# Kernel tuning notes

Measured on AMD Instinct MI355X. Metric: run time of the kernel, lower is better.

The kernel has to match this reference:

```python
import jax, jax.numpy as jnp
import numpy as np
import math

N_HEAD = 16

def setup_inputs() -> dict:
    key = jax.random.key(0)
    ks = jax.random.split(key, 8)
    B, S, P, NX = 4, 1024, 128, 1024
    return {
        "x": jax.random.normal(ks[0], (B, S, NX), jnp.float32),
        "M": jax.random.normal(ks[1], (B, P, NX), jnp.float32),
        "Mmask": jnp.ones((B, P), jnp.float32),
        "attention_mask": jnp.zeros((B, 1, 1, S), jnp.float32),
        "W_attn": jax.random.normal(ks[2], (NX, 3 * NX), jnp.float32) * 0.02,
        "b_attn": jnp.zeros((3 * NX,), jnp.float32),
        "W_mem": jax.random.normal(ks[3], (NX, 2 * NX), jnp.float32) * 0.02,
        "b_mem": jnp.zeros((2 * NX,), jnp.float32),
        "W_proj": jax.random.normal(ks[4], (NX, NX), jnp.float32) * 0.02,
        "b_proj": jnp.zeros((NX,), jnp.float32),
    }

def _split_heads(t, H):
    B, T, NX = t.shape
    return t.reshape(B, T, H, NX // H).transpose(0, 2, 1, 3)  # [B,H,T,dh]

def reference(x, M, Mmask, attention_mask, W_attn, b_attn, W_mem, b_mem, W_proj, b_proj):
    B, S, NX = x.shape
    H = N_HEAD
    dh = NX // H
    P = M.shape[1]

    # fused QKV projection (Conv1D == x @ W + b)
    qkv = x @ W_attn + b_attn
    q, k, v = jnp.split(qkv, 3, axis=2)

    # memory K/V projection, prepended along the key/value sequence axis
    ekv = M @ W_mem + b_mem
    ek, ev = jnp.split(ekv, 2, axis=2)
    key = jnp.concatenate([ek, k], axis=1)   # [B, P+S, NX]
    value = jnp.concatenate([ev, v], axis=1)

    qh = _split_heads(q, H)      # [B,H,S,dh]
    kh = _split_heads(key, H)    # [B,H,P+S,dh]
    vh = _split_heads(value, H)  # [B,H,P+S,dh]

    w = jnp.einsum('bhsd,bhtd->bhst', qh, kh) / math.sqrt(dh)  # [B,H,S,P+S]

    # causal bias over the self part, all-ones over the memory part
    causal = jnp.tril(jnp.ones((S, S), w.dtype))
    b = jnp.concatenate([jnp.ones((S, P), w.dtype), causal], axis=1)[None, None]  # [1,1,S,P+S]
    w = w * b - 10000.0 * (1.0 - b)

    # additive attention mask: memory-mask bias concatenated before token mask
    mem_bias = (1.0 - Mmask)[:, None, None, :] * -10000.0  # [B,1,1,P]
    am = jnp.concatenate([mem_bias, jnp.broadcast_to(attention_mask, (B, 1, 1, S))], axis=3)
    w = w + am

    w = jax.nn.softmax(w, axis=-1)
    a = jnp.einsum('bhst,bhtd->bhsd', w, vh)                  # [B,H,S,dh]
    a = a.transpose(0, 2, 1, 3).reshape(B, S, NX)             # merge heads
    return a @ W_proj + b_proj
```

## Files before the change

kernel.cpp:

```cpp
#include <hip/hip_runtime.h>
#include <hip/hip_bf16.h>


typedef __attribute__((ext_vector_type(8))) short bf16x8;
typedef __attribute__((ext_vector_type(4))) float f32x4;

#define MFMA16(a, b, c) __builtin_amdgcn_mfma_f32_16x16x32_bf16((a), (b), (c), 0, 0, 0)

#define GLOAD_LDS16(g, l)                                                  \
    __builtin_amdgcn_global_load_lds(                                      \
        (const __attribute__((address_space(1))) void*)(const void*)(g),   \
        (__attribute__((address_space(3))) void*)(void*)(l), 16, 0, 0)

static __device__ __forceinline__ unsigned short f2bf(float f) {
    union { float f; unsigned int u; } v; v.f = f;
    unsigned int u = v.u;
    return (unsigned short)((u + 0x7fffu + ((u >> 16) & 1u)) >> 16);
}

static __device__ __forceinline__ void transpose64(const float* __restrict__ W,
                                                   unsigned short* __restrict__ Wt,
                                                   int K, int N, int bx, int by,
                                                   float* tile ) {
    const int n0 = bx * 64, k0 = by * 64;
    const int tr = threadIdx.x >> 2, tc = (threadIdx.x & 3) * 16;
    #pragma unroll
    for (int i = 0; i < 4; i++) {
        float4 v = *(const float4*)&W[(size_t)(k0 + tr) * N + n0 + tc + i * 4];
        tile[tr * 65 + tc + i * 4 + 0] = v.x;
        tile[tr * 65 + tc + i * 4 + 1] = v.y;
        tile[tr * 65 + tc + i * 4 + 2] = v.z;
        tile[tr * 65 + tc + i * 4 + 3] = v.w;
    }
    __syncthreads();
    union { ushort4 u4[2]; unsigned short s[8]; } pk[2];
    #pragma unroll
    for (int half = 0; half < 2; half++)
        #pragma unroll
        for (int i = 0; i < 8; i++)
            pk[half].s[i] = f2bf(tile[(tc + half * 8 + i) * 65 + tr]);
    unsigned short* dst = &Wt[(size_t)(n0 + tr) * K + k0 + tc];
    *(ushort4*)(dst + 0) = pk[0].u4[0];
    *(ushort4*)(dst + 4) = pk[0].u4[1];
    *(ushort4*)(dst + 8) = pk[1].u4[0];
    *(ushort4*)(dst + 12) = pk[1].u4[1];
}

__global__ void prep_all(const float* __restrict__ x, const float* __restrict__ Mem,
                         unsigned short* __restrict__ x_bf, unsigned short* __restrict__ M_bf,
                         const float* __restrict__ W_attn, const float* __restrict__ W_mem,
                         const float* __restrict__ W_proj, unsigned short* __restrict__ Wat,
                         unsigned short* __restrict__ Wmt, unsigned short* __restrict__ Wpt,
                         const float* __restrict__ Mmask, const float* __restrict__ amask,
                         float* __restrict__ biasT) {
    __shared__ float tile[64 * 65];
    int bid = blockIdx.x;
    if (bid < 4608) {
        int i = bid * 256 + threadIdx.x;
        if (i < 1048576) {
            float4 v = ((const float4*)x)[i];
            ushort4 o; o.x = f2bf(v.x); o.y = f2bf(v.y); o.z = f2bf(v.z); o.w = f2bf(v.w);
            ((ushort4*)x_bf)[i] = o;
        } else {
            int j = i - 1048576;
            float4 v = ((const float4*)Mem)[j];
            ushort4 o; o.x = f2bf(v.x); o.y = f2bf(v.y); o.z = f2bf(v.z); o.w = f2bf(v.w);
            ((ushort4*)M_bf)[j] = o;
        }
        return;
    }
    bid -= 4608;
    if (bid < 768) {
        transpose64(W_attn, Wat, 1024, 3072, bid % 48, bid / 48, tile);
    } else if (bid < 1280) {
        int t = bid - 768;  transpose64(W_mem, Wmt, 1024, 2048, t % 32, t / 32, tile);
    } else if (bid < 1536) {
        int t = bid - 1280; transpose64(W_proj, Wpt, 1024, 1024, t % 16, t / 16, tile);
    } else {
        int i = (bid - 1536) * 256 + threadIdx.x;
        if (i < 4 * 1152) {
            int b = i / 1152, t = i % 1152;
            float v = (t < 128) ? (Mmask[b * 128 + t] - 1.f) * 10000.f
                                : amask[b * 1024 + t - 128];
            biasT[i] = v * 1.4426950408889634f;
        }
    }
}

__global__ __launch_bounds__(256, 4) void gemm_fused(
        const unsigned short* __restrict__ x_bf, const unsigned short* __restrict__ Wat,
        const float* __restrict__ b_attn, const unsigned short* __restrict__ M_bf,
        const unsigned short* __restrict__ Wmt, const float* __restrict__ b_mem,
        unsigned short* __restrict__ Qbuf, unsigned short* __restrict__ Kc,
        unsigned short* __restrict__ Vt) {
    __shared__ char smem[34816];
    unsigned short* As = (unsigned short*)smem;
    unsigned short* Bs = (unsigned short*)(smem + 8192);
    const int tid = threadIdx.x;
    const int lane = tid & 63, wave = tid >> 6;
    const int quad = lane >> 4, l16 = lane & 15;
    const int crow = lane >> 2, ccol = (lane & 3) * 8;
    const int bid = blockIdx.x;

    if (bid < 768) {
        const int bm = bid & 31, bn = bid >> 5;
        const int wm = (wave & 1) * 64, wn = (wave >> 1) * 64;
        const unsigned short* Abase = x_bf + (size_t)(bm * 128 + crow) * 1024 + ccol;
        const unsigned short* Bbase = Wat + (size_t)(bn * 128 + crow) * 1024 + ccol;
        f32x4 acc[4][4] = {};
        for (int k0 = 0; k0 < 1024; k0 += 32) {
            __syncthreads();
            #pragma unroll
            for (int cc = 0; cc < 4; cc++) {
                const int c = wave * 4 + cc;
                if (c < 8) GLOAD_LDS16(Abase + (size_t)(c * 16) * 1024 + k0, &As[c * 512]);
                else       GLOAD_LDS16(Bbase + (size_t)((c - 8) * 16) * 1024 + k0, &Bs[(c - 8) * 512]);
            }
            __syncthreads();
            bf16x8 af[4], bf[4];
            #pragma unroll
            for (int i = 0; i < 4; i++) af[i] = *(const bf16x8*)&As[(wm + i * 16 + l16) * 32 + quad * 8];
            #pragma unroll
            for (int j = 0; j < 4; j++) bf[j] = *(const bf16x8*)&Bs[(wn + j * 16 + l16) * 32 + quad * 8];
            #pragma unroll
            for (int i = 0; i < 4; i++)
                #pragma unroll
                for (int j = 0; j < 4; j++)
                    acc[i][j] = MFMA16(af[i], bf[j], acc[i][j]);
        }
        float bj[4];
        #pragma unroll
        for (int j = 0; j < 4; j++) bj[j] = b_attn[bn * 128 + wn + j * 16 + l16];
        __syncthreads();
        if (bn < 8) {
            #pragma unroll
            for (int i = 0; i < 4; i++) {
                const int row = bm * 128 + wm + i * 16 + quad * 4;
                #pragma unroll
                for (int j = 0; j < 4; j++) {
                    const int col = bn * 128 + wn + j * 16 + l16;
                    #pragma unroll
                    for (int r = 0; r < 4; r++)
                        Qbuf[(size_t)(row + r) * 1024 + col] = f2bf(acc[i][j][r] + bj[j]);
                }
            }
        } else if (bn < 16) {
            #pragma unroll
            for (int i = 0; i < 4; i++) {
                const int row = bm * 128 + wm + i * 16 + quad * 4;
                const int b = row >> 10, s = row & 1023;
                #pragma unroll
                for (int j = 0; j < 4; j++) {
                    const int c = bn * 128 + wn + j * 16 + l16 - 1024;
                    unsigned short* kd = Kc + (size_t)((b << 4) | (c >> 6)) * 73728 +
                                         (size_t)(s + 128) * 64 + (c & 63);
                    #pragma unroll
                    for (int r = 0; r < 4; r++) kd[(size_t)r * 64] = f2bf(acc[i][j][r] + bj[j]);
                }
            }
        } else {
            unsigned short* Tw = (unsigned short*)smem + wave * 4352;
            #pragma unroll
            for (int i = 0; i < 4; i++)
                #pragma unroll
                for (int j = 0; j < 4; j++)
                    #pragma unroll
                    for (int r = 0; r < 4; r++)
                        Tw[(j * 16 + l16) * 68 + i * 16 + quad * 4 + r] = f2bf(acc[i][j][r] + bj[j]);
            const int vb = (bn - 16) * 128 + wn;
            const int h = vb >> 6;
            const int b = bm >> 3, s0 = (bm * 128 + wm) & 1023;
            unsigned short* vd = Vt + (size_t)((b << 4) | h) * 73728 +
                                 (size_t)lane * 1152 + 128 + s0;
            #pragma unroll
            for (int ch = 0; ch < 8; ch++)
                *(bf16x8*)(vd + ch * 8) = *(const bf16x8*)&Tw[lane * 68 + ch * 8];
        }
    } else {
        const int t = bid - 768;
        const int bm = t >> 5, bn = t & 31;
        const int wm = (wave & 1) * 32, wn = (wave >> 1) * 32;
        const unsigned short* Abase = M_bf + (size_t)(bm * 64 + crow) * 1024 + ccol;
        const unsigned short* Bbase = Wmt + (size_t)(bn * 64 + crow) * 1024 + ccol;
        f32x4 acc[2][2] = {};
        for (int k0 = 0; k0 < 1024; k0 += 32) {
            __syncthreads();
            #pragma unroll
            for (int cc = 0; cc < 2; cc++) {
                const int c = wave * 2 + cc;
                if (c < 4) GLOAD_LDS16(Abase + (size_t)(c * 16) * 1024 + k0, &As[c * 512]);
                else       GLOAD_LDS16(Bbase + (size_t)((c - 4) * 16) * 1024 + k0, &Bs[(c - 4) * 512]);
            }
            __syncthreads();
            bf16x8 af[2], bf[2];
            #pragma unroll
            for (int i = 0; i < 2; i++) af[i] = *(const bf16x8*)&As[(wm + i * 16 + l16) * 32 + quad * 8];
            #pragma unroll
            for (int j = 0; j < 2; j++) bf[j] = *(const bf16x8*)&Bs[(wn + j * 16 + l16) * 32 + quad * 8];
            #pragma unroll
            for (int i = 0; i < 2; i++)
                #pragma unroll
                for (int j = 0; j < 2; j++)
                    acc[i][j] = MFMA16(af[i], bf[j], acc[i][j]);
        }
        float bj[2];
        #pragma unroll
        for (int j = 0; j < 2; j++) bj[j] = b_mem[bn * 64 + wn + j * 16 + l16];
        __syncthreads();
        if (bn < 16) {
            #pragma unroll
            for (int i = 0; i < 2; i++) {
                const int row = bm * 64 + wm + i * 16 + quad * 4;
                const int b = row >> 7, p = row & 127;
                #pragma unroll
                for (int j = 0; j < 2; j++) {
                    const int c = bn * 64 + wn + j * 16 + l16;
                    unsigned short* kd = Kc + (size_t)((b << 4) | (c >> 6)) * 73728 +
                                         (size_t)p * 64 + (c & 63);
                    #pragma unroll
                    for (int r = 0; r < 4; r++) kd[(size_t)r * 64] = f2bf(acc[i][j][r] + bj[j]);
                }
            }
        } else {
            unsigned short* Tw = (unsigned short*)smem + wave * 1152;
            #pragma unroll
            for (int i = 0; i < 2; i++)
                #pragma unroll
                for (int j = 0; j < 2; j++)
                    #pragma unroll
                    for (int r = 0; r < 4; r++)
                        Tw[(j * 16 + l16) * 36 + i * 16 + quad * 4 + r] = f2bf(acc[i][j][r] + bj[j]);
            const int vb = bn * 64 + wn - 1024;
            const int h = vb >> 6, d0 = vb & 63;
            const int b = (bm * 64 + wm) >> 7, p0 = (bm * 64 + wm) & 127;
            const int lc = lane >> 1, half = lane & 1;
            unsigned short* vd = Vt + (size_t)((b << 4) | h) * 73728 +
                                 (size_t)(d0 + lc) * 1152 + p0 + half * 16;
            #pragma unroll
            for (int ch = 0; ch < 2; ch++)
                *(bf16x8*)(vd + ch * 8) = *(const bf16x8*)&Tw[lc * 36 + half * 16 + ch * 8];
        }
    }
}

__global__ __launch_bounds__(128) void attn_kernel(const unsigned short* __restrict__ Qbuf,
                                                   const unsigned short* __restrict__ Kc,
                                                   const unsigned short* __restrict__ Vt,
                                                   const float* __restrict__ biasT,
                                                   unsigned short* __restrict__ Aout) {
    __shared__ unsigned short Ks[2][64 * 64];
    __shared__ unsigned short Vs[2][64 * 64];
    __shared__ unsigned short Ps[2][16 * 72];
    const int tid = threadIdx.x;
    const int lane = tid & 63, wave = tid >> 6;
    const int quad = lane >> 4, l16 = lane & 15;
    const int blk = blockIdx.x;
    const int xcd = blk & 7, idx = blk >> 3;
    const int bh = xcd * 8 + (idx & 7);
    const int pair = idx >> 3;
    const int h = bh & 15, b = bh >> 4;

    const unsigned short* Kb = Kc + (size_t)bh * 73728;
    const unsigned short* Vb = Vt + (size_t)bh * 73728;
    const float* bias_b = biasT + b * 1152;

    const int srow = lane >> 3;
    const int scol = ((lane & 7) ^ srow) * 8;
    const int rswz = l16 & 7;
    const int w32 = wave * 32;

#define STAGE_KV(t0_, kdst_, vdst_)                                            \
    {                                                                          \
        const unsigned short* gk = Kb + (size_t)((t0_) + w32 + srow) * 64 + scol; \
        const unsigned short* gv = Vb + (size_t)(w32 + srow) * 1152 + (t0_) + scol; \
        _Pragma("unroll")                                                      \
        for (int cc = 0; cc < 4; cc++) {                                       \
            GLOAD_LDS16(gk + (size_t)(cc * 8) * 64,   &(kdst_)[(w32 + cc * 8) * 64]); \
            GLOAD_LDS16(gv + (size_t)(cc * 8) * 1152, &(vdst_)[(w32 + cc * 8) * 64]); \
        }                                                                      \
    }

    bf16x8 ones;
    #pragma unroll
    for (int j = 0; j < 8; j++) ones[j] = (short)0x3F80;

    #pragma unroll
    for (int phase = 0; phase < 2; phase++) {
        const int qg = phase ? (31 - pair) : pair;
        const int qrow0 = qg * 32;
        const int qrow_w = qrow0 + wave * 16;

        bf16x8 qf[2];
        #pragma unroll
        for (int k2 = 0; k2 < 2; k2++)
            qf[k2] = *(const bf16x8*)(Qbuf + (size_t)(b * 1024 + qrow_w + l16) * 1024 +
                                      h * 64 + k2 * 32 + quad * 8);

        f32x4 o[4] = {};
        f32x4 oden = {};
        const int tmax = min(1152, ((qrow0 + 223) >> 6) << 6);

        STAGE_KV(0, Ks[0], Vs[0]);

        for (int t0 = 0; t0 < tmax; t0 += 64) {
            const int cur = (t0 >> 6) & 1;
            if (t0 + 64 < tmax) {
                if (cur) { STAGE_KV(t0 + 64, Ks[0], Vs[0]); }
                else     { STAGE_KV(t0 + 64, Ks[1], Vs[1]); }
                asm volatile("s_waitcnt vmcnt(8)\n\ts_barrier" ::: "memory");
            } else {
                asm volatile("s_waitcnt vmcnt(0)\n\ts_barrier" ::: "memory");
            }
            if (t0 <= qrow_w + 143) {
                const unsigned short* Kcur = Ks[cur];
                const unsigned short* Vcur = Vs[cur];
                const bool nomask = (t0 + 63 <= 128 + qrow_w);
                float4 bt[4];
                #pragma unroll
                for (int tn = 0; tn < 4; tn++)
                    bt[tn] = *(const float4*)(bias_b + t0 + tn * 16 + quad * 4);
                const int sg = qrow_w + l16;
                #pragma unroll
                for (int tn = 0; tn < 4; tn++) {
                    bf16x8 kf0 = *(const bf16x8*)&Kcur[(tn * 16 + l16) * 64 + (quad ^ rswz) * 8];
                    bf16x8 kf1 = *(const bf16x8*)&Kcur[(tn * 16 + l16) * 64 + ((quad + 4) ^ rswz) * 8];
                    f32x4 st = {};
                    st = MFMA16(kf0, qf[0], st);
                    st = MFMA16(kf1, qf[1], st);
                    float p[4];
                    #pragma unroll
                    for (int r = 0; r < 4; r++) {
                        float e = __builtin_amdgcn_exp2f(st[r] * 0.18033688011112042f + bt[tn][r]);
                        if (!nomask) {
                            const int tg = t0 + tn * 16 + quad * 4 + r;
                            e = (tg < 128 || tg - 128 <= sg) ? e : 0.f;
                        }
                        p[r] = e;
                    }
                    union { ushort4 u; __hip_bfloat162 h2[2]; } pk;
                    pk.h2[0] = __float22bfloat162_rn(float2{p[0], p[1]});
                    pk.h2[1] = __float22bfloat162_rn(float2{p[2], p[3]});
                    *(ushort4*)&Ps[wave][l16 * 72 + tn * 16 + quad * 4] = pk.u;
                }
                #pragma unroll
                for (int tk = 0; tk < 2; tk++) {
                    bf16x8 pf = *(const bf16x8*)&Ps[wave][l16 * 72 + tk * 32 + quad * 8];
                    oden = MFMA16(pf, ones, oden);
                    #pragma unroll
                    for (int dn = 0; dn < 4; dn++) {
                        bf16x8 vf = *(const bf16x8*)&Vcur[(dn * 16 + l16) * 64 +
                                                          ((tk * 4 + quad) ^ rswz) * 8];
                        o[dn] = MFMA16(pf, vf, o[dn]);
                    }
                }
            }
            asm volatile("s_barrier" ::: "memory");
        }

        #pragma unroll
        for (int r = 0; r < 4; r++) {
            const float inv = 1.f / oden[r];
            const size_t orow = (size_t)(b * 1024 + qrow_w + quad * 4 + r) * 1024 + h * 64;
            #pragma unroll
            for (int dn = 0; dn < 4; dn++)
                Aout[orow + dn * 16 + l16] = f2bf(o[dn][r] * inv);
        }
    }
#undef STAGE_KV
}

__global__ __launch_bounds__(256) void gemm_proj(const unsigned short* __restrict__ Abuf,
                                                 const unsigned short* __restrict__ Wpt,
                                                 const float* __restrict__ b_proj,
                                                 float* __restrict__ out) {
    __shared__ unsigned short As[128 * 32];
    __shared__ unsigned short Bs[64 * 32];
    const int tid = threadIdx.x;
    const int lane = tid & 63, wave = tid >> 6;
    const int quad = lane >> 4, l16 = lane & 15;
    const int wm = (wave & 1) * 64, wn = (wave >> 1) * 32;
    const int bm = blockIdx.x & 31, bn = blockIdx.x >> 5;
    const int crow = lane >> 2, ccol = (lane & 3) * 8;
    const unsigned short* Abase = Abuf + (size_t)(bm * 128 + crow) * 1024 + ccol;
    const unsigned short* Bbase = Wpt + (size_t)(bn * 64 + crow) * 1024 + ccol;

    f32x4 acc[4][2] = {};
    for (int k0 = 0; k0 < 1024; k0 += 32) {
        __syncthreads();
        #pragma unroll
        for (int cc = 0; cc < 3; cc++) {
            const int c = wave * 3 + cc;
            if (c < 8) GLOAD_LDS16(Abase + (size_t)(c * 16) * 1024 + k0, &As[c * 512]);
            else if (c < 12) GLOAD_LDS16(Bbase + (size_t)((c - 8) * 16) * 1024 + k0, &Bs[(c - 8) * 512]);
        }
        __syncthreads();
        bf16x8 af[4], bf[2];
        #pragma unroll
        for (int i = 0; i < 4; i++) af[i] = *(const bf16x8*)&As[(wm + i * 16 + l16) * 32 + quad * 8];
        #pragma unroll
        for (int j = 0; j < 2; j++) bf[j] = *(const bf16x8*)&Bs[(wn + j * 16 + l16) * 32 + quad * 8];
        #pragma unroll
        for (int i = 0; i < 4; i++)
            #pragma unroll
            for (int j = 0; j < 2; j++)
                acc[i][j] = MFMA16(af[i], bf[j], acc[i][j]);
    }
    float bj[2];
    #pragma unroll
    for (int j = 0; j < 2; j++) bj[j] = b_proj[bn * 64 + wn + j * 16 + l16];
    #pragma unroll
    for (int i = 0; i < 4; i++) {
        const int row = bm * 128 + wm + i * 16 + quad * 4;
        #pragma unroll
        for (int j = 0; j < 2; j++) {
            const int col = bn * 64 + wn + j * 16 + l16;
            #pragma unroll
            for (int r = 0; r < 4; r++)
                out[(size_t)(row + r) * 1024 + col] = acc[i][j][r] + bj[j];
        }
    }
}

extern "C" void kernel_launch(void* const* d_in, const int* in_sizes, int n_in,
                              void* d_out, int out_size, void* d_ws, size_t ws_size,
                              hipStream_t stream) {
    const float* x      = (const float*)d_in[0];
    const float* Mem    = (const float*)d_in[1];
    const float* Mmask  = (const float*)d_in[2];
    const float* amask  = (const float*)d_in[3];
    const float* W_attn = (const float*)d_in[4];
    const float* b_attn = (const float*)d_in[5];
    const float* W_mem  = (const float*)d_in[6];
    const float* b_mem  = (const float*)d_in[7];
    const float* W_proj = (const float*)d_in[8];
    const float* b_proj = (const float*)d_in[9];
    float* out = (float*)d_out;

    char* ws = (char*)d_ws;
    unsigned short* x_bf  = (unsigned short*)ws;  ws += (size_t)4096 * 1024 * 2;
    unsigned short* M_bf  = (unsigned short*)ws;  ws += (size_t)512 * 1024 * 2;
    unsigned short* Wat   = (unsigned short*)ws;  ws += (size_t)3072 * 1024 * 2;
    unsigned short* Wmt   = (unsigned short*)ws;  ws += (size_t)2048 * 1024 * 2;
    unsigned short* Wpt   = (unsigned short*)ws;  ws += (size_t)1024 * 1024 * 2;
    unsigned short* Qbuf  = (unsigned short*)ws;  ws += (size_t)4096 * 1024 * 2;
    unsigned short* Abuf  = (unsigned short*)ws;  ws += (size_t)4096 * 1024 * 2;
    unsigned short* Kc    = (unsigned short*)ws;  ws += (size_t)64 * 1152 * 64 * 2;
    unsigned short* Vt    = (unsigned short*)ws;  ws += (size_t)64 * 64 * 1152 * 2;
    float*          biasT = (float*)ws;           ws += (size_t)4 * 1152 * 4;

    prep_all<<<6163, 256, 0, stream>>>(x, Mem, x_bf, M_bf, W_attn, W_mem, W_proj,
                                       Wat, Wmt, Wpt, Mmask, amask, biasT);
    gemm_fused<<<1024, 256, 0, stream>>>(x_bf, Wat, b_attn, M_bf, Wmt, b_mem,
                                         Qbuf, Kc, Vt);
    attn_kernel<<<1024, 128, 0, stream>>>(Qbuf, Kc, Vt, biasT, Abuf);
    gemm_proj<<<512, 256, 0, stream>>>(Abuf, Wpt, b_proj, out);
}
```

Measured before the change: 198.4 us.

## Rewrite QKV/memory GEMM with 256x256 tiles, double-buffered swizzled LDS pipeline

Replaces the 128x128 (QKV) and 64x64 (memory) GEMM tiles with a single 256x256-tile, 512-thread kernel that uses K=64 steps, a double-buffered LDS with an XOR swizzle, and prefetching of the next K slice interleaved with the MFMA phases. It also uses s_setprio around MFMAs and remaps block IDs across XCDs. The aim is more data reuse per LDS load, fewer bank conflicts, and global loads that overlap compute. In exchange the grid shrinks to 208 blocks, which may underfill a 256-CU device, and register pressure rises with 128 accumulators per thread.

```diff
diff --git a/kernel.cpp b/kernel.cpp
--- a/kernel.cpp
+++ b/kernel.cpp
@@ -87,158 +87,181 @@
     }
 }
 
-__global__ __launch_bounds__(256, 4) void gemm_fused(
+__global__ __launch_bounds__(512, 2) void gemm_fused(
         const unsigned short* __restrict__ x_bf, const unsigned short* __restrict__ Wat,
         const float* __restrict__ b_attn, const unsigned short* __restrict__ M_bf,
         const unsigned short* __restrict__ Wmt, const float* __restrict__ b_mem,
         unsigned short* __restrict__ Qbuf, unsigned short* __restrict__ Kc,
         unsigned short* __restrict__ Vt) {
-    __shared__ char smem[34816];
-    unsigned short* As = (unsigned short*)smem;
-    unsigned short* Bs = (unsigned short*)(smem + 8192);
+    __shared__ unsigned short lds[2][32768];
     const int tid = threadIdx.x;
     const int lane = tid & 63, wave = tid >> 6;
     const int quad = lane >> 4, l16 = lane & 15;
-    const int crow = lane >> 2, ccol = (lane & 3) * 8;
-    const int bid = blockIdx.x;
-
-    if (bid < 768) {
-        const int bm = bid & 31, bn = bid >> 5;
-        const int wm = (wave & 1) * 64, wn = (wave >> 1) * 64;
-        const unsigned short* Abase = x_bf + (size_t)(bm * 128 + crow) * 1024 + ccol;
-        const unsigned short* Bbase = Wat + (size_t)(bn * 128 + crow) * 1024 + ccol;
-        f32x4 acc[4][4] = {};
-        for (int k0 = 0; k0 < 1024; k0 += 32) {
-            __syncthreads();
-            #pragma unroll
-            for (int cc = 0; cc < 4; cc++) {
-                const int c = wave * 4 + cc;
-                if (c < 8) GLOAD_LDS16(Abase + (size_t)(c * 16) * 1024 + k0, &As[c * 512]);
-                else       GLOAD_LDS16(Bbase + (size_t)((c - 8) * 16) * 1024 + k0, &Bs[(c - 8) * 512]);
-            }
-            __syncthreads();
-            bf16x8 af[4], bf[4];
-            #pragma unroll
-            for (int i = 0; i < 4; i++) af[i] = *(const bf16x8*)&As[(wm + i * 16 + l16) * 32 + quad * 8];
-            #pragma unroll
-            for (int j = 0; j < 4; j++) bf[j] = *(const bf16x8*)&Bs[(wn + j * 16 + l16) * 32 + quad * 8];
-            #pragma unroll
-            for (int i = 0; i < 4; i++)
+    const int l7 = l16 & 7;
+    const int srow = lane >> 3;
+    const int sblk = (lane & 7) ^ srow;
+    const int wrow = wave * 16;
+    const int wm = (wave & 1) * 128;
+    const int wn = (wave >> 1) * 64;
+
+    int tm, tn;
+    const unsigned short *Ab, *Bb;
+    const float* bias;
+    bool qkv;
+    if (blockIdx.x < 192) {
+        const int nb = (blockIdx.x & 7) * 24 + (blockIdx.x >> 3);
+        tm = nb & 15; tn = nb >> 4;
+        Ab = x_bf; Bb = Wat; bias = b_attn; qkv = true;
+    } else {
+        const int e = blockIdx.x - 192;
+        tm = e >> 3; tn = e & 7;
+        Ab = M_bf; Bb = Wmt; bias = b_mem; qkv = false;
+    }
+    const int Mrow0 = tm * 256, Nrow0 = tn * 256;
+
+#define STG(slot, dstoff, srcp, row0, kt1)                                     \
+    { _Pragma("unroll")                                                        \
+      for (int c = 0; c < 2; c++)                                              \
+          GLOAD_LDS16((srcp) + (size_t)((row0) + wrow + c * 8 + srow) * 1024 + \
+                          (kt1) * 64 + sblk * 8,                               \
+                      &lds[slot][(dstoff) + (wrow + c * 8) * 64]); }
+
+    STG(0, 16384, Bb, Nrow0, 0); STG(0, 24576, Bb, Nrow0 + 128, 0);
+    STG(0, 0,     Ab, Mrow0, 0); STG(0, 8192,  Ab, Mrow0 + 128, 0);
+    asm volatile("s_waitcnt vmcnt(0)\n\ts_barrier" ::: "memory");
+
+    f32x4 acc[8][4] = {};
+    for (int kt = 0; kt < 16; kt++) {
+        const int s = kt & 1, nx = s ^ 1;
+        bf16x8 bfr[4][2];
+        #pragma unroll
+        for (int p = 0; p < 4; p++) {
+            bf16x8 af[2][2];
+            #pragma unroll
+            for (int k = 0; k < 2; k++)
+                #pragma unroll
+                for (int ks = 0; ks < 2; ks++)
+                    af[k][ks] = *(const bf16x8*)&lds[s][(wm + (2 * p + k) * 16 + l16) * 64 +
+                                                       (((ks * 4 + quad) ^ l7) * 8)];
+            if (p == 0) {
                 #pragma unroll
                 for (int j = 0; j < 4; j++)
-                    acc[i][j] = MFMA16(af[i], bf[j], acc[i][j]);
-        }
-        float bj[4];
-        #pragma unroll
-        for (int j = 0; j < 4; j++) bj[j] = b_attn[bn * 128 + wn + j * 16 + l16];
-        __syncthreads();
-        if (bn < 8) {
-            #pragma unroll
-            for (int i = 0; i < 4; i++) {
-                const int row = bm * 128 + wm + i * 16 + quad * 4;
+                    #pragma unroll
+                    for (int ks = 0; ks < 2; ks++)
+                        bfr[j][ks] = *(const bf16x8*)&lds[s][16384 + (wn + j * 16 + l16) * 64 +
+                                                            (((ks * 4 + quad) ^ l7) * 8)];
+            }
+            if (kt < 15) {
+                if (p == 0) { STG(nx, 16384, Bb, Nrow0, kt + 1);
+                              STG(nx, 24576, Bb, Nrow0 + 128, kt + 1); }
+                else if (p == 1) { STG(nx, 0,    Ab, Mrow0, kt + 1); }
+                else if (p == 2) { STG(nx, 8192, Ab, Mrow0 + 128, kt + 1); }
+            }
+            if (p == 3) asm volatile("s_waitcnt vmcnt(0)\n\ts_barrier" ::: "memory");
+            else        asm volatile("s_barrier" ::: "memory");
+            __builtin_amdgcn_s_setprio(1);
+            #pragma unroll
+            for (int k = 0; k < 2; k++)
                 #pragma unroll
                 for (int j = 0; j < 4; j++) {
-                    const int col = bn * 128 + wn + j * 16 + l16;
+                    acc[2 * p + k][j] = MFMA16(af[k][0], bfr[j][0], acc[2 * p + k][j]);
+                    acc[2 * p + k][j] = MFMA16(af[k][1], bfr[j][1], acc[2 * p + k][j]);
+                }
+            __builtin_amdgcn_s_setprio(0);
+            asm volatile("s_barrier" ::: "memory");
+        }
+    }
+#undef STG
+    __syncthreads();
+
+    float bj[4];
+    #pragma unroll
+    for (int j = 0; j < 4; j++) bj[j] = bias[Nrow0 + wn + j * 16 + l16];
+
+    if (qkv) {
+        const int b = tm >> 2;
+        const int sb = (tm & 3) * 256 + wm;
+        if (tn < 4) {
+            #pragma unroll
+            for (int i = 0; i < 8; i++) {
+                const int row = Mrow0 + wm + i * 16 + quad * 4;
+                #pragma unroll
+                for (int j = 0; j < 4; j++) {
+                    const int col = Nrow0 + wn + j * 16 + l16;
                     #pragma unroll
                     for (int r = 0; r < 4; r++)
                         Qbuf[(size_t)(row + r) * 1024 + col] = f2bf(acc[i][j][r] + bj[j]);
                 }
             }
-        } else if (bn < 16) {
-            #pragma unroll
-            for (int i = 0; i < 4; i++) {
-                const int row = bm * 128 + wm + i * 16 + quad * 4;
-                const int b = row >> 10, s = row & 1023;
+        } else if (tn < 8) {
+            const int cb = (tn - 4) * 256 + wn;
+            unsigned short* kb2 = Kc + (size_t)((b << 4) | (cb >> 6)) * 73728;
+            #pragma unroll
+            for (int i = 0; i < 8; i++) {
+                const int s0 = sb + i * 16 + quad * 4;
                 #pragma unroll
                 for (int j = 0; j < 4; j++) {
-                    const int c = bn * 128 + wn + j * 16 + l16 - 1024;
-                    unsigned short* kd = Kc + (size_t)((b << 4) | (c >> 6)) * 73728 +
-                                         (size_t)(s + 128) * 64 + (c & 63);
-                    #pragma unroll
-                    for (int r = 0; r < 4; r++) kd[(size_t)r * 64] = f2bf(acc[i][j][r] + bj[j]);
+                    const int d = j * 16 + l16;
+                    #pragma unroll
+                    for (int r = 0; r < 4; r++)
+                        kb2[(size_t)(128 + s0 + r) * 64 + d] = f2bf(acc[i][j][r] + bj[j]);
                 }
             }
         } else {
-            unsigned short* Tw = (unsigned short*)smem + wave * 4352;
-            #pragma unroll
-            for (int i = 0; i < 4; i++)
-                #pragma unroll
-                for (int j = 0; j < 4; j++)
+            const int vb = (tn - 8) * 256 + wn;
+            unsigned short* Tw = &lds[0][0] + wave * 4352;
+            unsigned short* vdb = Vt + (size_t)((b << 4) | (vb >> 6)) * 73728;
+            #pragma unroll
+            for (int hf = 0; hf < 2; hf++) {
+                #pragma unroll
+                for (int i2 = 0; i2 < 4; i2++)
+                    #pragma unroll
+                    for (int j = 0; j < 4; j++)
+                        #pragma unroll
+                        for (int r = 0; r < 4; r++)
+                            Tw[(j * 16 + l16) * 68 + i2 * 16 + quad * 4 + r] =
+                                f2bf(acc[hf * 4 + i2][j][r] + bj[j]);
+                unsigned short* vd = vdb + (size_t)lane * 1152 + 128 + sb + hf * 64;
+                #pragma unroll
+                for (int ch = 0; ch < 8; ch++)
+                    *(bf16x8*)(vd + ch * 8) = *(const bf16x8*)&Tw[lane * 68 + ch * 8];
+            }
+        }
+    } else {
+        const int b = (Mrow0 + wm) >> 7;
+        if (tn < 4) {
+            const int cb = tn * 256 + wn;
+            unsigned short* kb2 = Kc + (size_t)((b << 4) | (cb >> 6)) * 73728;
+            #pragma unroll
+            for (int i = 0; i < 8; i++) {
+                const int p0 = i * 16 + quad * 4;
+                #pragma unroll
+                for (int j = 0; j < 4; j++) {
+                    const int d = j * 16 + l16;
                     #pragma unroll
                     for (int r = 0; r < 4; r++)
-                        Tw[(j * 16 + l16) * 68 + i * 16 + quad * 4 + r] = f2bf(acc[i][j][r] + bj[j]);
-            const int vb = (bn - 16) * 128 + wn;
-            const int h = vb >> 6;
-            const int b = bm >> 3, s0 = (bm * 128 + wm) & 1023;
-            unsigned short* vd = Vt + (size_t)((b << 4) | h) * 73728 +
-                                 (size_t)lane * 1152 + 128 + s0;
-            #pragma unroll
-            for (int ch = 0; ch < 8; ch++)
-                *(bf16x8*)(vd + ch * 8) = *(const bf16x8*)&Tw[lane * 68 + ch * 8];
-        }
-    } else {
-        const int t = bid - 768;
-        const int bm = t >> 5, bn = t & 31;
-        const int wm = (wave & 1) * 32, wn = (wave >> 1) * 32;
-        const unsigned short* Abase = M_bf + (size_t)(bm * 64 + crow) * 1024 + ccol;
-        const unsigned short* Bbase = Wmt + (size_t)(bn * 64 + crow) * 1024 + ccol;
-        f32x4 acc[2][2] = {};
-        for (int k0 = 0; k0 < 1024; k0 += 32) {
-            __syncthreads();
-            #pragma unroll
-            for (int cc = 0; cc < 2; cc++) {
-                const int c = wave * 2 + cc;
-                if (c < 4) GLOAD_LDS16(Abase + (size_t)(c * 16) * 1024 + k0, &As[c * 512]);
-                else       GLOAD_LDS16(Bbase + (size_t)((c - 4) * 16) * 1024 + k0, &Bs[(c - 4) * 512]);
-            }
-            __syncthreads();
-            bf16x8 af[2], bf[2];
-            #pragma unroll
-            for (int i = 0; i < 2; i++) af[i] = *(const bf16x8*)&As[(wm + i * 16 + l16) * 32 + quad * 8];
-            #pragma unroll
-            for (int j = 0; j < 2; j++) bf[j] = *(const bf16x8*)&Bs[(wn + j * 16 + l16) * 32 + quad * 8];
-            #pragma unroll
-            for (int i = 0; i < 2; i++)
-                #pragma unroll
-                for (int j = 0; j < 2; j++)
-                    acc[i][j] = MFMA16(af[i], bf[j], acc[i][j]);
-        }
-        float bj[2];
-        #pragma unroll
-        for (int j = 0; j < 2; j++) bj[j] = b_mem[bn * 64 + wn + j * 16 + l16];
-        __syncthreads();
-        if (bn < 16) {
-            #pragma unroll
-            for (int i = 0; i < 2; i++) {
-                const int row = bm * 64 + wm + i * 16 + quad * 4;
-                const int b = row >> 7, p = row & 127;
-                #pragma unroll
-                for (int j = 0; j < 2; j++) {
-                    const int c = bn * 64 + wn + j * 16 + l16;
-                    unsigned short* kd = Kc + (size_t)((b << 4) | (c >> 6)) * 73728 +
-                                         (size_t)p * 64 + (c & 63);
-                    #pragma unroll
-                    for (int r = 0; r < 4; r++) kd[(size_t)r * 64] = f2bf(acc[i][j][r] + bj[j]);
+                        kb2[(size_t)(p0 + r) * 64 + d] = f2bf(acc[i][j][r] + bj[j]);
                 }
             }
         } else {
-            unsigned short* Tw = (unsigned short*)smem + wave * 1152;
-            #pragma unroll
-            for (int i = 0; i < 2; i++)
-                #pragma unroll
-                for (int j = 0; j < 2; j++)
-                    #pragma unroll
-                    for (int r = 0; r < 4; r++)
-                        Tw[(j * 16 + l16) * 36 + i * 16 + quad * 4 + r] = f2bf(acc[i][j][r] + bj[j]);
-            const int vb = bn * 64 + wn - 1024;
-            const int h = vb >> 6, d0 = vb & 63;
-            const int b = (bm * 64 + wm) >> 7, p0 = (bm * 64 + wm) & 127;
-            const int lc = lane >> 1, half = lane & 1;
-            unsigned short* vd = Vt + (size_t)((b << 4) | h) * 73728 +
-                                 (size_t)(d0 + lc) * 1152 + p0 + half * 16;
-            #pragma unroll
-            for (int ch = 0; ch < 2; ch++)
-                *(bf16x8*)(vd + ch * 8) = *(const bf16x8*)&Tw[lc * 36 + half * 16 + ch * 8];
+            const int vb = (tn - 4) * 256 + wn;
+            unsigned short* Tw = &lds[0][0] + wave * 4352;
+            unsigned short* vdb = Vt + (size_t)((b << 4) | (vb >> 6)) * 73728;
+            #pragma unroll
+            for (int hf = 0; hf < 2; hf++) {
+                #pragma unroll
+                for (int i2 = 0; i2 < 4; i2++)
+                    #pragma unroll
+                    for (int j = 0; j < 4; j++)
+                        #pragma unroll
+                        for (int r = 0; r < 4; r++)
+                            Tw[(j * 16 + l16) * 68 + i2 * 16 + quad * 4 + r] =
+                                f2bf(acc[hf * 4 + i2][j][r] + bj[j]);
+                unsigned short* vd = vdb + (size_t)lane * 1152 + hf * 64;
+                #pragma unroll
+                for (int ch = 0; ch < 8; ch++)
+                    *(bf16x8*)(vd + ch * 8) = *(const bf16x8*)&Tw[lane * 68 + ch * 8];
+            }
         }
     }
 }
@@ -450,8 +473,8 @@
 
     prep_all<<<6163, 256, 0, stream>>>(x, Mem, x_bf, M_bf, W_attn, W_mem, W_proj,
                                        Wat, Wmt, Wpt, Mmask, amask, biasT);
-    gemm_fused<<<1024, 256, 0, stream>>>(x_bf, Wat, b_attn, M_bf, Wmt, b_mem,
-                                         Qbuf, Kc, Vt);
+    gemm_fused<<<208, 512, 0, stream>>>(x_bf, Wat, b_attn, M_bf, Wmt, b_mem,
+                                        Qbuf, Kc, Vt);
     attn_kernel<<<1024, 128, 0, stream>>>(Qbuf, Kc, Vt, biasT, Abuf);
     gemm_proj<<<512, 256, 0, stream>>>(Abuf, Wpt, b_proj, out);
 }
```

New measurement: 197.8 us. About the same (-0.3%).
